# Kernel tuning notes

Measured on AMD Instinct MI355X. Metric: run time of the kernel, lower is better.

Reference implementation:

```python
import jax, jax.numpy as jnp
import numpy as np
import math

N_HEAD = 12

def setup_inputs() -> dict:
    key = jax.random.key(0)
    ks = jax.random.split(key, 4)
    B, T, C = 4, 2048, 768
    x = jax.random.normal(ks[0], (B, T, C), dtype=jnp.float32)
    W_attn = jax.random.normal(ks[1], (C, 3 * C), dtype=jnp.float32) * (1.0 / math.sqrt(C))
    b_attn = jnp.zeros((3 * C,), dtype=jnp.float32)
    W_proj = jax.random.normal(ks[2], (C, C), dtype=jnp.float32) * (1.0 / math.sqrt(C))
    b_proj = jnp.zeros((C,), dtype=jnp.float32)
    decay_rates = jnp.full((N_HEAD,), 0.05, dtype=jnp.float32)
    return {"x": x, "W_attn": W_attn, "b_attn": b_attn,
            "W_proj": W_proj, "b_proj": b_proj, "decay_rates": decay_rates}

def reference(x, W_attn, b_attn, W_proj, b_proj, decay_rates):
    B, T, C = x.shape
    H = N_HEAD
    D = C // H
    qkv = x @ W_attn + b_attn                      # [B,T,3C]
    q, k, v = jnp.split(qkv, 3, axis=-1)
    q = q.reshape(B, T, H, D).transpose(0, 2, 1, 3)  # [B,H,T,D]
    k = k.reshape(B, T, H, D).transpose(0, 2, 1, 3)
    v = v.reshape(B, T, H, D).transpose(0, 2, 1, 3)
    att = jnp.einsum('bhqd,bhkd->bhqk', q, k) * (1.0 / math.sqrt(D))
    i = jnp.arange(T)[:, None]
    j = jnp.arange(T)[None, :]
    causal = i >= j                                  # [T,T]
    att = jnp.where(causal[None, None], att, -jnp.inf)
    att = jax.nn.softmax(att, axis=-1)
    # distances buffer: tril(j - i).abs() == (i - j) on the lower triangle, 0 above
    dist = jnp.where(causal, (i - j).astype(jnp.float32), 0.0)  # [T,T]
    decay = jnp.exp(-decay_rates[None, :, None, None] * dist[None, None])  # [1,H,T,T]
    att = att * decay
    att = att / (jnp.sum(att, axis=-1, keepdims=True) + 1e-8)
    y = jnp.einsum('bhqk,bhkd->bhqd', att, v)        # [B,H,T,D]
    y = y.transpose(0, 2, 1, 3).reshape(B, T, C)
    return y @ W_proj + b_proj
```

## Files before the change

kernel.cpp:

```cpp
#include <hip/hip_runtime.h>
#include <hip/hip_bf16.h>
#include <math.h>

#define T_ 2048
#define C_ 768
#define H_ 12
#define D_ 64
#define M_ 8192
#define QKV_N 2304

typedef short bf16x8 __attribute__((ext_vector_type(8)));
typedef float f32x4 __attribute__((ext_vector_type(4)));
typedef unsigned short u16;
typedef u16 u16x8 __attribute__((ext_vector_type(8)));
typedef u16 u16x4 __attribute__((ext_vector_type(4)));

__device__ u16 g_xb [M_*C_];
__device__ u16 g_wat[QKV_N*C_];
__device__ u16 g_wpt[C_*C_];
__device__ u16 g_q [M_*C_];
__device__ u16 g_k [M_*C_];
__device__ u16 g_vt[M_*C_];
__device__ u16 g_y [M_*C_];

__device__ __forceinline__ u16 f2bf(float f) {
    return __bfloat16_as_ushort(__float2bfloat16(f));
}
__device__ __forceinline__ f32x4 mfma16(bf16x8 a, bf16x8 b, f32x4 c) {
    return __builtin_amdgcn_mfma_f32_16x16x32_bf16(a, b, c, 0, 0, 0);
}
__device__ __forceinline__ int swz(int row, int col) {
    return row*64 + ((((col >> 3) ^ (row & 7))) << 3) + (col & 7);
}

__global__ __launch_bounds__(256) void k_prep_x(const float* __restrict__ x)
{
    const int idx = blockIdx.x*256 + threadIdx.x;
    float4 a = ((const float4*)x)[idx*2];
    float4 b = ((const float4*)x)[idx*2+1];
    u16x8 o;
    o[0]=f2bf(a.x); o[1]=f2bf(a.y); o[2]=f2bf(a.z); o[3]=f2bf(a.w);
    o[4]=f2bf(b.x); o[5]=f2bf(b.y); o[6]=f2bf(b.z); o[7]=f2bf(b.w);
    ((u16x8*)g_xb)[idx] = o;
}

__global__ __launch_bounds__(256) void k_prep_wt(const float* __restrict__ src,
                                                 int which, int K, int N)
{
    __shared__ u16 L[64][72];
    const int tid = threadIdx.x;
    const int n0 = blockIdx.x*64, k0 = blockIdx.y*64;
    u16* dst = which ? g_wpt : g_wat;

    const int r  = tid >> 2;
    const int c0 = (tid & 3) * 16;
    const float* p = &src[(size_t)(k0 + r)*N + n0 + c0];
    float4 v[4];
    #pragma unroll
    for (int c = 0; c < 4; ++c) v[c] = ((const float4*)p)[c];
    const float* vf = (const float*)v;
    #pragma unroll
    for (int j = 0; j < 16; ++j) L[c0 + j][r] = f2bf(vf[j]);
    __syncthreads();
    const int nn = tid >> 2;
    const int s  = (tid & 3) * 16;
    *(u16x8*)&dst[(size_t)(n0+nn)*K + k0 + s]     = *(const u16x8*)&L[nn][s];
    *(u16x8*)&dst[(size_t)(n0+nn)*K + k0 + s + 8] = *(const u16x8*)&L[nn][s+8];
}

__global__ __launch_bounds__(256) void k_qkv(const float* __restrict__ bias)
{
    __shared__ u16 As[128][40];
    __shared__ u16 Bs[128][40];

    const int tid  = threadIdx.x;
    const int lane = tid & 63;
    const int wid  = tid >> 6;
    const int l15  = lane & 15;
    const int lg   = lane >> 4;
    const int wm = wid >> 1, wn = wid & 1;
    const int m0 = blockIdx.x * 128;
    const int n0 = blockIdx.y * 128;

    const int sr = tid >> 2;
    const int sc = (tid & 3) * 8;

    f32x4 acc[4][4];
    #pragma unroll
    for (int i = 0; i < 4; ++i)
        #pragma unroll
        for (int j = 0; j < 4; ++j) acc[i][j] = (f32x4){0.f,0.f,0.f,0.f};

    for (int k0 = 0; k0 < C_; k0 += 32) {
        u16x8 a0 = *(const u16x8*)&g_xb [(size_t)(m0+sr    )*C_ + k0 + sc];
        u16x8 a1 = *(const u16x8*)&g_xb [(size_t)(m0+sr+64 )*C_ + k0 + sc];
        u16x8 b0 = *(const u16x8*)&g_wat[(size_t)(n0+sr    )*C_ + k0 + sc];
        u16x8 b1 = *(const u16x8*)&g_wat[(size_t)(n0+sr+64 )*C_ + k0 + sc];
        __syncthreads();
        *(u16x8*)&As[sr   ][sc] = a0;
        *(u16x8*)&As[sr+64][sc] = a1;
        *(u16x8*)&Bs[sr   ][sc] = b0;
        *(u16x8*)&Bs[sr+64][sc] = b1;
        __syncthreads();

        bf16x8 bfr[4];
        #pragma unroll
        for (int nt = 0; nt < 4; ++nt)
            bfr[nt] = *(const bf16x8*)&Bs[wn*64 + nt*16 + l15][lg*8];
        #pragma unroll
        for (int mt = 0; mt < 4; ++mt) {
            bf16x8 afr = *(const bf16x8*)&As[wm*64 + mt*16 + l15][lg*8];
            #pragma unroll
            for (int nt = 0; nt < 4; ++nt)
                acc[mt][nt] = mfma16(afr, bfr[nt], acc[mt][nt]);
        }
    }

    const int nb    = n0 + wn*64;
    const int which = nb / C_;
    const int h     = (nb % C_) / D_;
    const int mbase = m0 + wm*64;
    const int bb    = mbase >> 11;
    const int bh    = bb*H_ + h;
    float bv4[4];
    #pragma unroll
    for (int nt = 0; nt < 4; ++nt) bv4[nt] = bias[nb + nt*16 + l15];

    if (which == 2) {
        #pragma unroll
        for (int mt = 0; mt < 4; ++mt) {
            const int tb = (mbase + mt*16 + lg*4) & (T_-1);
            #pragma unroll
            for (int nt = 0; nt < 4; ++nt) {
                const int d = nt*16 + l15;
                u16x4 pk;
                #pragma unroll
                for (int r = 0; r < 4; ++r) pk[r] = f2bf(acc[mt][nt][r] + bv4[nt]);
                *(u16x4*)&g_vt[((size_t)bh*D_ + d)*T_ + tb] = pk;
            }
        }
    } else {
        u16* dst = which ? g_k : g_q;
        #pragma unroll
        for (int mt = 0; mt < 4; ++mt)
            #pragma unroll
            for (int r = 0; r < 4; ++r) {
                const int t = (mbase + mt*16 + lg*4 + r) & (T_-1);
                #pragma unroll
                for (int nt = 0; nt < 4; ++nt)
                    dst[((size_t)bh*T_ + t)*D_ + nt*16 + l15] = f2bf(acc[mt][nt][r] + bv4[nt]);
            }
    }
}

__global__ __launch_bounds__(256) void k_attn(const float* __restrict__ rates)
{
    __shared__ u16 Ks[64*64];
    __shared__ u16 Vt[64*64];
    __shared__ u16 Ps[4][16*64];

    const int tid  = threadIdx.x;
    const int lane = tid & 63;
    const int wid  = tid >> 6;
    const int l15  = lane & 15;
    const int lg   = lane >> 4;

    const int id  = blockIdx.x;
    const int bh  = (id & 7)*6 + ((id >> 3) % 6);
    const int qt  = 31 - ((id >> 3) / 6);
    const int h   = bh % H_;
    const int bb  = bh / H_;
    const float rate = rates[h];
    const float LOG2E  = 1.4426950408889634f;
    const float srate  = rate * LOG2E;
    const float sscale = 0.125f * LOG2E;

    const int i0  = qt * 64;
    const int thr = wid*16 + l15;
    const int ig  = i0 + thr;

    const int wt = (int)(34.4f / (fmaxf(rate, 1e-8f) * 64.0f)) + 2;
    const int nT = min(qt + 1, wt);

    const u16* qb  = &g_q [(size_t)bh*T_*D_];
    const u16* kb  = &g_k [(size_t)bh*T_*D_];
    const u16* vtb = &g_vt[(size_t)bh*D_*T_];

    bf16x8 qf[2];
    qf[0] = *(const bf16x8*)&qb[(size_t)ig*D_ + lg*8];
    qf[1] = *(const bf16x8*)&qb[(size_t)ig*D_ + 32 + lg*8];

    float joff[16];
    #pragma unroll
    for (int t = 0; t < 4; ++t)
        #pragma unroll
        for (int r = 0; r < 4; ++r) joff[t*4+r] = srate * (float)(t*16 + lg*4 + r);

    f32x4 oAcc[4];
    #pragma unroll
    for (int n = 0; n < 4; ++n) oAcc[n] = (f32x4){0.f,0.f,0.f,0.f};
    float den = 0.f, mrow = 0.f;

    const int srow = tid >> 2;
    const int sc   = (tid & 3) << 4;

    u16x8 kp0 = *(const u16x8*)&kb[(size_t)(i0+srow)*D_ + sc];
    u16x8 kp1 = *(const u16x8*)&kb[(size_t)(i0+srow)*D_ + sc + 8];
    u16x8 vp0 = *(const u16x8*)&vtb[(size_t)srow*T_ + i0 + sc];
    u16x8 vp1 = *(const u16x8*)&vtb[(size_t)srow*T_ + i0 + sc + 8];

    u16* PsW = &Ps[wid][0];

    for (int tt = 0; tt < nT; ++tt) {
        const int j0 = i0 - tt*64;
        __syncthreads();
        *(u16x8*)&Ks[swz(srow, sc)]     = kp0;
        *(u16x8*)&Ks[swz(srow, sc + 8)] = kp1;
        *(u16x8*)&Vt[swz(srow, sc)]     = vp0;
        *(u16x8*)&Vt[swz(srow, sc + 8)] = vp1;
        __syncthreads();
        if (tt + 1 < nT) {
            const int jn = j0 - 64;
            kp0 = *(const u16x8*)&kb[(size_t)(jn+srow)*D_ + sc];
            kp1 = *(const u16x8*)&kb[(size_t)(jn+srow)*D_ + sc + 8];
            vp0 = *(const u16x8*)&vtb[(size_t)srow*T_ + jn + sc];
            vp1 = *(const u16x8*)&vtb[(size_t)srow*T_ + jn + sc + 8];
        }

        __builtin_amdgcn_s_setprio(1);
        f32x4 sAcc[4];
        #pragma unroll
        for (int t = 0; t < 4; ++t) sAcc[t] = (f32x4){0.f,0.f,0.f,0.f};
        #pragma unroll
        for (int t = 0; t < 4; ++t)
            #pragma unroll
            for (int kf = 0; kf < 2; ++kf) {
                bf16x8 kfr = *(const bf16x8*)&Ks[swz(t*16 + l15, kf*32 + lg*8)];
                sAcc[t] = mfma16(kfr, qf[kf], sAcc[t]);
            }
        __builtin_amdgcn_s_setprio(0);

        float e[16];
        if (tt == 0) {
            const float sth = srate * (float)thr;
            float pv[16];
            float mx = -3e38f;
            #pragma unroll
            for (int t = 0; t < 4; ++t)
                #pragma unroll
                for (int r = 0; r < 4; ++r) {
                    const int jj = t*16 + lg*4 + r;
                    float v = fmaf(sAcc[t][r], sscale, joff[t*4+r] - sth);
                    if (jj > thr) v = -3e38f;
                    pv[t*4+r] = v;
                    mx = fmaxf(mx, v);
                }
            mx = fmaxf(mx, __shfl_xor(mx, 16, 64));
            mx = fmaxf(mx, __shfl_xor(mx, 32, 64));
            mrow = mx;
            #pragma unroll
            for (int i = 0; i < 16; ++i) {
                e[i] = __builtin_amdgcn_exp2f(pv[i] - mx);
                den += e[i];
            }
        } else {
            const float c0m = fmaf(srate, (float)(j0 - ig), -mrow);
            #pragma unroll
            for (int t = 0; t < 4; ++t)
                #pragma unroll
                for (int r = 0; r < 4; ++r) {
                    const float v = fmaf(sAcc[t][r], sscale, c0m + joff[t*4+r]);
                    const float p = __builtin_amdgcn_exp2f(v);
                    e[t*4+r] = p;
                    den += p;
                }
        }

        #pragma unroll
        for (int t = 0; t < 4; ++t) {
            u16x4 pk = { f2bf(e[t*4]), f2bf(e[t*4+1]), f2bf(e[t*4+2]), f2bf(e[t*4+3]) };
            *(u16x4*)&PsW[swz(l15, t*16 + lg*4)] = pk;
        }

        __builtin_amdgcn_s_setprio(1);
        #pragma unroll
        for (int kf = 0; kf < 2; ++kf) {
            bf16x8 pa = *(const bf16x8*)&PsW[swz(l15, kf*32 + lg*8)];
            #pragma unroll
            for (int n = 0; n < 4; ++n) {
                bf16x8 vf = *(const bf16x8*)&Vt[swz(n*16 + l15, kf*32 + lg*8)];
                oAcc[n] = mfma16(pa, vf, oAcc[n]);
            }
        }
        __builtin_amdgcn_s_setprio(0);
    }

    den += __shfl_xor(den, 16, 64);
    den += __shfl_xor(den, 32, 64);
    const float inv = 1.f / den;
    float ivr[4];
    #pragma unroll
    for (int r = 0; r < 4; ++r) ivr[r] = __shfl(inv, lg*4 + r, 64);
    #pragma unroll
    for (int r = 0; r < 4; ++r) {
        const int row = i0 + wid*16 + lg*4 + r;
        #pragma unroll
        for (int n = 0; n < 4; ++n)
            g_y[(size_t)(bb*T_ + row)*C_ + h*D_ + n*16 + l15] = f2bf(oAcc[n][r] * ivr[r]);
    }
}

__global__ __launch_bounds__(256) void k_proj(const float* __restrict__ bias,
                                              float* __restrict__ out)
{
    __shared__ u16 As[128][40];
    __shared__ u16 Bs[128][40];

    const int tid  = threadIdx.x;
    const int lane = tid & 63;
    const int wid  = tid >> 6;
    const int l15  = lane & 15;
    const int lg   = lane >> 4;
    const int wm = wid >> 1, wn = wid & 1;
    const int m0 = blockIdx.x * 128;
    const int n0 = blockIdx.y * 128;

    const int sr = tid >> 2;
    const int sc = (tid & 3) * 8;

    f32x4 acc[4][4];
    #pragma unroll
    for (int i = 0; i < 4; ++i)
        #pragma unroll
        for (int j = 0; j < 4; ++j) acc[i][j] = (f32x4){0.f,0.f,0.f,0.f};

    for (int k0 = 0; k0 < C_; k0 += 32) {
        u16x8 a0 = *(const u16x8*)&g_y  [(size_t)(m0+sr   )*C_ + k0 + sc];
        u16x8 a1 = *(const u16x8*)&g_y  [(size_t)(m0+sr+64)*C_ + k0 + sc];
        u16x8 b0 = *(const u16x8*)&g_wpt[(size_t)(n0+sr   )*C_ + k0 + sc];
        u16x8 b1 = *(const u16x8*)&g_wpt[(size_t)(n0+sr+64)*C_ + k0 + sc];
        __syncthreads();
        *(u16x8*)&As[sr   ][sc] = a0;
        *(u16x8*)&As[sr+64][sc] = a1;
        *(u16x8*)&Bs[sr   ][sc] = b0;
        *(u16x8*)&Bs[sr+64][sc] = b1;
        __syncthreads();

        bf16x8 bfr[4];
        #pragma unroll
        for (int nt = 0; nt < 4; ++nt)
            bfr[nt] = *(const bf16x8*)&Bs[wn*64 + nt*16 + l15][lg*8];
        #pragma unroll
        for (int mt = 0; mt < 4; ++mt) {
            bf16x8 afr = *(const bf16x8*)&As[wm*64 + mt*16 + l15][lg*8];
            #pragma unroll
            for (int nt = 0; nt < 4; ++nt)
                acc[mt][nt] = mfma16(afr, bfr[nt], acc[mt][nt]);
        }
    }

    float bv4[4];
    #pragma unroll
    for (int nt = 0; nt < 4; ++nt) bv4[nt] = bias[n0 + wn*64 + nt*16 + l15];
    #pragma unroll
    for (int mt = 0; mt < 4; ++mt)
        #pragma unroll
        for (int r = 0; r < 4; ++r) {
            const int m = m0 + wm*64 + mt*16 + lg*4 + r;
            #pragma unroll
            for (int nt = 0; nt < 4; ++nt)
                out[(size_t)m*C_ + n0 + wn*64 + nt*16 + l15] = acc[mt][nt][r] + bv4[nt];
        }
}

extern "C" void kernel_launch(void* const* d_in, const int* in_sizes, int n_in,
                              void* d_out, int out_size, void* d_ws, size_t ws_size,
                              hipStream_t stream) {
    (void)in_sizes; (void)n_in; (void)d_ws; (void)ws_size; (void)out_size;
    const float* x      = (const float*)d_in[0];
    const float* W_attn = (const float*)d_in[1];
    const float* b_attn = (const float*)d_in[2];
    const float* W_proj = (const float*)d_in[3];
    const float* b_proj = (const float*)d_in[4];
    const float* rates  = (const float*)d_in[5];

    hipLaunchKernelGGL(k_prep_x,  dim3(M_*C_/8/256), dim3(256), 0, stream, x);
    hipLaunchKernelGGL(k_prep_wt, dim3(QKV_N/64, C_/64), dim3(256), 0, stream, W_attn, 0, C_, QKV_N);
    hipLaunchKernelGGL(k_prep_wt, dim3(C_/64,    C_/64), dim3(256), 0, stream, W_proj, 1, C_, C_);
    hipLaunchKernelGGL(k_qkv,  dim3(M_/128, QKV_N/128), dim3(256), 0, stream, b_attn);
    hipLaunchKernelGGL(k_attn, dim3(1536),              dim3(256), 0, stream, rates);
    hipLaunchKernelGGL(k_proj, dim3(M_/128, C_/128),    dim3(256), 0, stream, b_proj, (float*)d_out);
}
```

Baseline: 219.0 us.

## Load GEMM and attention tiles directly to LDS via global_load_lds with XOR swizzle

```diff
diff --git a/kernel.cpp b/kernel.cpp
--- a/kernel.cpp
+++ b/kernel.cpp
@@ -29,6 +29,14 @@
 __device__ __forceinline__ f32x4 mfma16(bf16x8 a, bf16x8 b, f32x4 c) {
     return __builtin_amdgcn_mfma_f32_16x16x32_bf16(a, b, c, 0, 0, 0);
 }
+__device__ __forceinline__ void gl16(const u16* g, u16* l) {
+    __builtin_amdgcn_global_load_lds(
+        (const __attribute__((address_space(1))) unsigned int*)g,
+        (__attribute__((address_space(3))) unsigned int*)l, 16, 0, 0);
+}
+__device__ __forceinline__ int ridx(int row, int chunk) {
+    return row*64 + (((chunk) ^ (row & 7)) << 3);
+}
 __device__ __forceinline__ int swz(int row, int col) {
     return row*64 + ((((col >> 3) ^ (row & 7))) << 3) + (col & 7);
 }
@@ -70,8 +78,8 @@
 
 __global__ __launch_bounds__(256) void k_qkv(const float* __restrict__ bias)
 {
-    __shared__ u16 As[128][40];
-    __shared__ u16 Bs[128][40];
+    __shared__ u16 As[128*64];
+    __shared__ u16 Bs[128*64];
 
     const int tid  = threadIdx.x;
     const int lane = tid & 63;
@@ -82,8 +90,8 @@
     const int m0 = blockIdx.x * 128;
     const int n0 = blockIdx.y * 128;
 
-    const int sr = tid >> 2;
-    const int sc = (tid & 3) * 8;
+    const int srow8 = lane >> 3;
+    const int schk  = (lane & 7) ^ srow8;
 
     f32x4 acc[4][4];
     #pragma unroll
@@ -91,28 +99,31 @@
         #pragma unroll
         for (int j = 0; j < 4; ++j) acc[i][j] = (f32x4){0.f,0.f,0.f,0.f};
 
-    for (int k0 = 0; k0 < C_; k0 += 32) {
-        u16x8 a0 = *(const u16x8*)&g_xb [(size_t)(m0+sr    )*C_ + k0 + sc];
-        u16x8 a1 = *(const u16x8*)&g_xb [(size_t)(m0+sr+64 )*C_ + k0 + sc];
-        u16x8 b0 = *(const u16x8*)&g_wat[(size_t)(n0+sr    )*C_ + k0 + sc];
-        u16x8 b1 = *(const u16x8*)&g_wat[(size_t)(n0+sr+64 )*C_ + k0 + sc];
-        __syncthreads();
-        *(u16x8*)&As[sr   ][sc] = a0;
-        *(u16x8*)&As[sr+64][sc] = a1;
-        *(u16x8*)&Bs[sr   ][sc] = b0;
-        *(u16x8*)&Bs[sr+64][sc] = b1;
-        __syncthreads();
-
-        bf16x8 bfr[4];
-        #pragma unroll
-        for (int nt = 0; nt < 4; ++nt)
-            bfr[nt] = *(const bf16x8*)&Bs[wn*64 + nt*16 + l15][lg*8];
-        #pragma unroll
-        for (int mt = 0; mt < 4; ++mt) {
-            bf16x8 afr = *(const bf16x8*)&As[wm*64 + mt*16 + l15][lg*8];
-            #pragma unroll
-            for (int nt = 0; nt < 4; ++nt)
-                acc[mt][nt] = mfma16(afr, bfr[nt], acc[mt][nt]);
+    for (int k0 = 0; k0 < C_; k0 += 64) {
+        __syncthreads();
+        #pragma unroll
+        for (int i = 0; i < 4; ++i) {
+            const int r = wid*32 + i*8;
+            gl16(&g_xb [(size_t)(m0 + r + srow8)*C_ + k0 + (schk<<3)], &As[r*64]);
+            gl16(&g_wat[(size_t)(n0 + r + srow8)*C_ + k0 + (schk<<3)], &Bs[r*64]);
+        }
+        __syncthreads();
+        #pragma unroll
+        for (int kf = 0; kf < 2; ++kf) {
+            bf16x8 bfr[4];
+            #pragma unroll
+            for (int nt = 0; nt < 4; ++nt) {
+                const int rw = wn*64 + nt*16 + l15;
+                bfr[nt] = *(const bf16x8*)&Bs[ridx(rw, kf*4 + lg)];
+            }
+            #pragma unroll
+            for (int mt = 0; mt < 4; ++mt) {
+                const int rw = wm*64 + mt*16 + l15;
+                bf16x8 afr = *(const bf16x8*)&As[ridx(rw, kf*4 + lg)];
+                #pragma unroll
+                for (int nt = 0; nt < 4; ++nt)
+                    acc[mt][nt] = mfma16(afr, bfr[nt], acc[mt][nt]);
+            }
         }
     }
 
@@ -201,31 +212,21 @@
     for (int n = 0; n < 4; ++n) oAcc[n] = (f32x4){0.f,0.f,0.f,0.f};
     float den = 0.f, mrow = 0.f;
 
-    const int srow = tid >> 2;
-    const int sc   = (tid & 3) << 4;
-
-    u16x8 kp0 = *(const u16x8*)&kb[(size_t)(i0+srow)*D_ + sc];
-    u16x8 kp1 = *(const u16x8*)&kb[(size_t)(i0+srow)*D_ + sc + 8];
-    u16x8 vp0 = *(const u16x8*)&vtb[(size_t)srow*T_ + i0 + sc];
-    u16x8 vp1 = *(const u16x8*)&vtb[(size_t)srow*T_ + i0 + sc + 8];
+    const int srow8 = lane >> 3;
+    const int schk  = (lane & 7) ^ srow8;
 
     u16* PsW = &Ps[wid][0];
 
     for (int tt = 0; tt < nT; ++tt) {
         const int j0 = i0 - tt*64;
         __syncthreads();
-        *(u16x8*)&Ks[swz(srow, sc)]     = kp0;
-        *(u16x8*)&Ks[swz(srow, sc + 8)] = kp1;
-        *(u16x8*)&Vt[swz(srow, sc)]     = vp0;
-        *(u16x8*)&Vt[swz(srow, sc + 8)] = vp1;
-        __syncthreads();
-        if (tt + 1 < nT) {
-            const int jn = j0 - 64;
-            kp0 = *(const u16x8*)&kb[(size_t)(jn+srow)*D_ + sc];
-            kp1 = *(const u16x8*)&kb[(size_t)(jn+srow)*D_ + sc + 8];
-            vp0 = *(const u16x8*)&vtb[(size_t)srow*T_ + jn + sc];
-            vp1 = *(const u16x8*)&vtb[(size_t)srow*T_ + jn + sc + 8];
-        }
+        #pragma unroll
+        for (int i = 0; i < 2; ++i) {
+            const int r = wid*16 + i*8;
+            gl16(&kb [(size_t)(j0 + r + srow8)*D_ + (schk<<3)], &Ks[r*64]);
+            gl16(&vtb[(size_t)(r + srow8)*T_ + j0 + (schk<<3)], &Vt[r*64]);
+        }
+        __syncthreads();
 
         __builtin_amdgcn_s_setprio(1);
         f32x4 sAcc[4];
@@ -235,7 +236,7 @@
         for (int t = 0; t < 4; ++t)
             #pragma unroll
             for (int kf = 0; kf < 2; ++kf) {
-                bf16x8 kfr = *(const bf16x8*)&Ks[swz(t*16 + l15, kf*32 + lg*8)];
+                bf16x8 kfr = *(const bf16x8*)&Ks[ridx(t*16 + l15, kf*4 + lg)];
                 sAcc[t] = mfma16(kfr, qf[kf], sAcc[t]);
             }
         __builtin_amdgcn_s_setprio(0);
@@ -285,10 +286,10 @@
         __builtin_amdgcn_s_setprio(1);
         #pragma unroll
         for (int kf = 0; kf < 2; ++kf) {
-            bf16x8 pa = *(const bf16x8*)&PsW[swz(l15, kf*32 + lg*8)];
+            bf16x8 pa = *(const bf16x8*)&PsW[ridx(l15, kf*4 + lg)];
             #pragma unroll
             for (int n = 0; n < 4; ++n) {
-                bf16x8 vf = *(const bf16x8*)&Vt[swz(n*16 + l15, kf*32 + lg*8)];
+                bf16x8 vf = *(const bf16x8*)&Vt[ridx(n*16 + l15, kf*4 + lg)];
                 oAcc[n] = mfma16(pa, vf, oAcc[n]);
             }
         }
@@ -313,8 +314,8 @@
 __global__ __launch_bounds__(256) void k_proj(const float* __restrict__ bias,
                                               float* __restrict__ out)
 {
-    __shared__ u16 As[128][40];
-    __shared__ u16 Bs[128][40];
+    __shared__ u16 As[128*64];
+    __shared__ u16 Bs[128*64];
 
     const int tid  = threadIdx.x;
     const int lane = tid & 63;
@@ -325,8 +326,8 @@
     const int m0 = blockIdx.x * 128;
     const int n0 = blockIdx.y * 128;
 
-    const int sr = tid >> 2;
-    const int sc = (tid & 3) * 8;
+    const int srow8 = lane >> 3;
+    const int schk  = (lane & 7) ^ srow8;
 
     f32x4 acc[4][4];
     #pragma unroll
@@ -334,28 +335,31 @@
         #pragma unroll
         for (int j = 0; j < 4; ++j) acc[i][j] = (f32x4){0.f,0.f,0.f,0.f};
 
-    for (int k0 = 0; k0 < C_; k0 += 32) {
-        u16x8 a0 = *(const u16x8*)&g_y  [(size_t)(m0+sr   )*C_ + k0 + sc];
-        u16x8 a1 = *(const u16x8*)&g_y  [(size_t)(m0+sr+64)*C_ + k0 + sc];
-        u16x8 b0 = *(const u16x8*)&g_wpt[(size_t)(n0+sr   )*C_ + k0 + sc];
-        u16x8 b1 = *(const u16x8*)&g_wpt[(size_t)(n0+sr+64)*C_ + k0 + sc];
-        __syncthreads();
-        *(u16x8*)&As[sr   ][sc] = a0;
-        *(u16x8*)&As[sr+64][sc] = a1;
-        *(u16x8*)&Bs[sr   ][sc] = b0;
-        *(u16x8*)&Bs[sr+64][sc] = b1;
-        __syncthreads();
-
-        bf16x8 bfr[4];
-        #pragma unroll
-        for (int nt = 0; nt < 4; ++nt)
-            bfr[nt] = *(const bf16x8*)&Bs[wn*64 + nt*16 + l15][lg*8];
-        #pragma unroll
-        for (int mt = 0; mt < 4; ++mt) {
-            bf16x8 afr = *(const bf16x8*)&As[wm*64 + mt*16 + l15][lg*8];
-            #pragma unroll
-            for (int nt = 0; nt < 4; ++nt)
-                acc[mt][nt] = mfma16(afr, bfr[nt], acc[mt][nt]);
+    for (int k0 = 0; k0 < C_; k0 += 64) {
+        __syncthreads();
+        #pragma unroll
+        for (int i = 0; i < 4; ++i) {
+            const int r = wid*32 + i*8;
+            gl16(&g_y  [(size_t)(m0 + r + srow8)*C_ + k0 + (schk<<3)], &As[r*64]);
+            gl16(&g_wpt[(size_t)(n0 + r + srow8)*C_ + k0 + (schk<<3)], &Bs[r*64]);
+        }
+        __syncthreads();
+        #pragma unroll
+        for (int kf = 0; kf < 2; ++kf) {
+            bf16x8 bfr[4];
+            #pragma unroll
+            for (int nt = 0; nt < 4; ++nt) {
+                const int rw = wn*64 + nt*16 + l15;
+                bfr[nt] = *(const bf16x8*)&Bs[ridx(rw, kf*4 + lg)];
+            }
+            #pragma unroll
+            for (int mt = 0; mt < 4; ++mt) {
+                const int rw = wm*64 + mt*16 + l15;
+                bf16x8 afr = *(const bf16x8*)&As[ridx(rw, kf*4 + lg)];
+                #pragma unroll
+                for (int nt = 0; nt < 4; ++nt)
+                    acc[mt][nt] = mfma16(afr, bfr[nt], acc[mt][nt]);
+            }
         }
     }
 
```

Result: faster. 206.2 us (-5.8%).
